# Optimization experiments

Hardware: AMD Instinct MI355X
Metric: run time of the kernel (lower is better)

Reference implementation:

```python
import math
import jax, jax.numpy as jnp
import numpy as np

HID = 2048      # hidden_size
NH = 16         # num_heads
KD = HID // NH  # key head dim = 128 (even, required by XPOS)
VD = HID        # value_dim (value_factor=1)
VHD = VD // NH  # value head dim
SCALE_BASE = 512
ROPE_BASE = 10000.0
GN_EPS = 1e-5


def _rotate_every_two(x):
    x1 = x[..., ::2]
    x2 = x[..., 1::2]
    return jnp.stack((-x2, x1), axis=-1).reshape(x.shape)


def _dup(a):  # repeat_interleave(x, 2, dim=-1)
    return jnp.repeat(a, 2, axis=-1)


def _xpos_apply(x, pos, inv_freq, xpos_scale, downscale):
    # x: [B, H, S, KD], pos: [B, S]
    posf = pos.astype(jnp.float32)
    angles = posf[:, :, None] * inv_freq[None, None, :]          # [B, S, KD/2]
    sin = _dup(jnp.sin(angles))[:, None]                          # [B, 1, S, KD]
    cos = _dup(jnp.cos(angles))[:, None]
    scale = xpos_scale[None, None, :] ** (posf[:, :, None] / SCALE_BASE)
    if downscale:
        scale = 1.0 / scale
    scale = _dup(scale)[:, None]                                  # [B, 1, S, KD]
    return (x * cos + _rotate_every_two(x) * sin) * scale


def setup_inputs() -> dict:
    key = jax.random.key(0)
    ks = jax.random.split(key, 6)
    B, S = 1, 2048
    std = 1.0 / HID
    x = jax.random.normal(ks[0], (B, S, HID), dtype=jnp.float32)
    position_ids = jnp.broadcast_to(jnp.arange(S, dtype=jnp.int64), (B, S))
    Wq = jax.random.normal(ks[1], (HID, HID), dtype=jnp.float32) * std
    Wk = jax.random.normal(ks[2], (HID, HID), dtype=jnp.float32) * std
    Wv = jax.random.normal(ks[3], (HID, VD), dtype=jnp.float32) * std
    Wg = jax.random.normal(ks[4], (HID, VD), dtype=jnp.float32) * std
    Wo = jax.random.normal(ks[5], (VD, HID), dtype=jnp.float32) * std
    gn_weight = jnp.ones((VD,), dtype=jnp.float32)
    gn_bias = jnp.zeros((VD,), dtype=jnp.float32)
    return {"x": x, "position_ids": position_ids, "Wq": Wq, "Wk": Wk,
            "Wv": Wv, "Wg": Wg, "Wo": Wo,
            "gn_weight": gn_weight, "gn_bias": gn_bias}


def reference(x, position_ids, Wq, Wk, Wv, Wg, Wo, gn_weight, gn_bias):
    B, S, _ = x.shape
    # XPOS / multiscale-decay buffers (deterministic, as in XPOSRelativePosition)
    inv_freq = 1.0 / (ROPE_BASE ** (jnp.arange(0, KD, 2, dtype=jnp.float32) / KD))
    xpos_scale = (jnp.arange(0, KD, 2, dtype=jnp.float32) + 0.4 * KD) / (1.4 * KD)
    gamma = 1.0 - jnp.exp(jnp.linspace(math.log(1.0 / 32), math.log(1.0 / 512), NH))
    log_gamma = jnp.log(gamma)                                    # [NH]

    # projections -> [B, H, S, d]
    q = (x @ Wq).reshape(B, S, NH, KD).transpose(0, 2, 1, 3)
    k = (x @ Wk).reshape(B, S, NH, KD).transpose(0, 2, 1, 3)
    v = (x @ Wv).reshape(B, S, NH, VHD).transpose(0, 2, 1, 3)
    g = x @ Wg                                                    # [B, S, VD]

    q = _xpos_apply(q, position_ids, inv_freq, xpos_scale, downscale=False)
    k = _xpos_apply(k, position_ids, inv_freq, xpos_scale, downscale=True)

    # decay mask: exp(log_gamma * (i-j)) for i>=j else 0   [B, H, S, S]
    relpos = position_ids[:, :, None] - position_ids[:, None, :]  # [B, S, S]
    decay = jnp.exp(log_gamma[None, :, None, None]
                    * jnp.maximum(relpos, 0)[:, None].astype(jnp.float32))
    decay = decay * (relpos >= 0)[:, None].astype(jnp.float32)

    scores = jnp.einsum('bhqd,bhkd->bhqk', q, k) * decay          # [B, H, S, S]
    retained = jnp.einsum('bhqk,bhkv->bhqv', scores, v)           # [B, H, S, VHD]

    # GroupNorm(num_heads, value_dim): normalize each head group per token
    r = retained.transpose(0, 2, 1, 3)                            # [B, S, H, VHD]
    mean = r.mean(axis=-1, keepdims=True)
    var = r.var(axis=-1, keepdims=True)
    rn = (r - mean) * jax.lax.rsqrt(var + GN_EPS)
    rn = rn * gn_weight.reshape(NH, VHD) + gn_bias.reshape(NH, VHD)
    rn = rn.reshape(B, S, VD)

    out = (jax.nn.silu(g) * rn) @ Wo                              # [B, S, HID]
    return out
```

## Files before the change

### kernel.cpp

```cpp
#include <hip/hip_runtime.h>
#include <math.h>

#define S_LEN 2048
#define HIDD  2048
#define NHEAD 16
#define HD    128

#define TILE_SH 4096

typedef __attribute__((ext_vector_type(8))) short short8;
typedef __attribute__((ext_vector_type(4))) float float4v;
typedef unsigned short ushort_t;

static __device__ __forceinline__ ushort_t f2bf(float f) {
    unsigned int u = __float_as_uint(f);
    u += 0x7fff + ((u >> 16) & 1);
    return (ushort_t)(u >> 16);
}
static __device__ __forceinline__ float bf2f(ushort_t s) {
    return __uint_as_float(((unsigned int)s) << 16);
}
__device__ __forceinline__ float silu_f(float x) { return x / (1.f + expf(-x)); }

__device__ __forceinline__ void gl_lds16(const ushort_t* g, short* l) {
    __builtin_amdgcn_global_load_lds((const __attribute__((address_space(1))) void*)g,
                                     (__attribute__((address_space(3))) void*)l, 16, 0, 0);
}

__global__ __launch_bounds__(256)
void split_kernel(const float* __restrict__ in, ushort_t* __restrict__ hi,
                  ushort_t* __restrict__ lo, int n4)
{
    const int i = blockIdx.x * 256 + threadIdx.x;
    if (i >= n4) return;
    const float4 v = ((const float4*)in)[i];
    ushort4 h, l;
    h.x = f2bf(v.x); l.x = f2bf(v.x - bf2f(h.x));
    h.y = f2bf(v.y); l.y = f2bf(v.y - bf2f(h.y));
    h.z = f2bf(v.z); l.z = f2bf(v.z - bf2f(h.z));
    h.w = f2bf(v.w); l.w = f2bf(v.w - bf2f(h.w));
    const int row = i >> 9, c4 = (i & 511) * 4;
    const size_t off = ((size_t)((row >> 7) * 64 + (c4 >> 5))) * TILE_SH
                     + (row & 127) * 32 + (c4 & 31);
    *(ushort4*)&hi[off] = h;
    *(ushort4*)&lo[off] = l;
}

__global__ __launch_bounds__(256)
void addp_kernel(float* __restrict__ out, const float* __restrict__ p, int n4)
{
    const int i = blockIdx.x * 256 + threadIdx.x;
    if (i >= n4) return;
    float4 a = ((const float4*)out)[i];
    const float4 b = ((const float4*)p)[i];
    a.x += b.x; a.y += b.y; a.z += b.z; a.w += b.w;
    ((float4*)out)[i] = a;
}

__global__ __launch_bounds__(256)
void split_transpose(const float* __restrict__ W, ushort_t* __restrict__ Thi,
                     ushort_t* __restrict__ Tlo)
{
    __shared__ float t[64][65];
    const int k0 = blockIdx.y * 64, n0 = blockIdx.x * 64;
    const int tx = threadIdx.x & 15, ty = threadIdx.x >> 4;
    #pragma unroll
    for (int it = 0; it < 4; it++) {
        const int k = ty + it * 16;
        const float4 v = *(const float4*)&W[(size_t)(k0 + k) * HIDD + n0 + tx * 4];
        t[k][tx * 4 + 0] = v.x; t[k][tx * 4 + 1] = v.y;
        t[k][tx * 4 + 2] = v.z; t[k][tx * 4 + 3] = v.w;
    }
    __syncthreads();
    #pragma unroll
    for (int it = 0; it < 4; it++) {
        const int n = ty + it * 16;
        ushort4 h, l; float a;
        a = t[tx * 4 + 0][n]; h.x = f2bf(a); l.x = f2bf(a - bf2f(h.x));
        a = t[tx * 4 + 1][n]; h.y = f2bf(a); l.y = f2bf(a - bf2f(h.y));
        a = t[tx * 4 + 2][n]; h.z = f2bf(a); l.z = f2bf(a - bf2f(h.z));
        a = t[tx * 4 + 3][n]; h.w = f2bf(a); l.w = f2bf(a - bf2f(h.w));
        const int nn_ = n0 + n, kk_ = k0 + tx * 4;
        const size_t off = ((size_t)((nn_ >> 7) * 64 + (kk_ >> 5))) * TILE_SH
                         + (nn_ & 127) * 32 + (kk_ & 31);
        *(ushort4*)&Thi[off] = h;
        *(ushort4*)&Tlo[off] = l;
    }
}

template<int MODE>
__global__ __launch_bounds__(256, 2)
void mfma_gemm(const ushort_t* __restrict__ Ahi, const ushort_t* __restrict__ Alo,
               const ushort_t* __restrict__ WT, const int* __restrict__ pos_ids,
               ushort_t* __restrict__ qhi, ushort_t* __restrict__ qlo,
               ushort_t* __restrict__ khi, ushort_t* __restrict__ klo,
               ushort_t* __restrict__ vThi, ushort_t* __restrict__ vTlo,
               float* __restrict__ gbuf, float* __restrict__ outC)
{
    __shared__ __align__(16) short sm[(MODE == 1) ? 32768 : 16384];

    const int tid = threadIdx.x;
    const int w = tid >> 6, L = tid & 63;
    const int qd = L >> 4, lc = L & 15;
    const int lin = blockIdx.x;
    int n0, m0, kh = 0;
    if (MODE == 0) {
        n0 = (((lin & 7) << 3) + ((lin >> 3) & 7)) << 7;
        m0 = (lin >> 6) << 7;
    } else {
        n0 = (lin & 15) << 7;
        m0 = ((lin >> 4) & 15) << 7;
        kh = lin >> 8;
    }
    const size_t PL = (size_t)HIDD * HIDD;

    int sel, nn;
    const ushort_t *Bhi, *Blo;
    if (MODE == 0) {
        sel = n0 >> 11; nn = n0 & 2047;
        Bhi = WT + (size_t)sel * 2 * PL; Blo = Bhi + PL;
    } else {
        sel = -1; nn = n0;
        Bhi = WT; Blo = WT + PL;
    }

    const ushort_t* pbase = (w == 0) ? Ahi : (w == 1) ? Alo : (w == 2) ? Bhi : Blo;
    const int rt = ((w < 2) ? m0 : nn) >> 7;
    const ushort_t* tb0 = pbase + (size_t)rt * 64 * TILE_SH + L * 8;

    const int wm = (w & 1) * 64, wn = (w >> 1) * 64;
    int aoff[4], boff[4];
    #pragma unroll
    for (int i = 0; i < 4; i++) aoff[i] = (wm + i * 16 + lc) * 32 + qd * 8;
    #pragma unroll
    for (int j = 0; j < 4; j++) boff[j] = (wn + j * 16 + lc) * 32 + qd * 8;

    float4v acc[4][4];
    #pragma unroll
    for (int i = 0; i < 4; i++)
        #pragma unroll
        for (int j = 0; j < 4; j++)
            #pragma unroll
            for (int r = 0; r < 4; r++) acc[i][j][r] = 0.f;

    const int kt0 = (MODE == 1) ? kh * 32 : 0;
    const int kt1 = (MODE == 1) ? kt0 + 32 : 64;

    if (MODE == 0) {
        short* ldsw = sm + w * 4096;
        for (int kt = kt0; kt < kt1; kt++) {
            const ushort_t* g = tb0 + (size_t)kt * TILE_SH;
            #pragma unroll
            for (int t = 0; t < 8; t++)
                gl_lds16(g + t * 512, ldsw + t * 512);
            __syncthreads();

            short8 bhf[4], blf[4];
            #pragma unroll
            for (int j = 0; j < 4; j++) {
                bhf[j] = *(const short8*)(sm + 8192  + boff[j]);
                blf[j] = *(const short8*)(sm + 12288 + boff[j]);
            }
            #pragma unroll
            for (int i = 0; i < 4; i++) {
                const short8 ahf = *(const short8*)(sm + aoff[i]);
                const short8 alf = *(const short8*)(sm + 4096 + aoff[i]);
                #pragma unroll
                for (int j = 0; j < 4; j++) {
                    acc[i][j] = __builtin_amdgcn_mfma_f32_16x16x32_bf16(ahf, bhf[j], acc[i][j], 0, 0, 0);
                    acc[i][j] = __builtin_amdgcn_mfma_f32_16x16x32_bf16(alf, bhf[j], acc[i][j], 0, 0, 0);
                    acc[i][j] = __builtin_amdgcn_mfma_f32_16x16x32_bf16(ahf, blf[j], acc[i][j], 0, 0, 0);
                }
            }
            __syncthreads();
        }
    } else {
        {
            const ushort_t* g = tb0 + (size_t)kt0 * TILE_SH;
            #pragma unroll
            for (int t = 0; t < 8; t++)
                gl_lds16(g + t * 512, sm + w * 4096 + t * 512);
            asm volatile("s_waitcnt vmcnt(0)" ::: "memory");
            __builtin_amdgcn_s_barrier();
            __builtin_amdgcn_sched_barrier(0);
        }
        int cur = 0;
        for (int kt = kt0; kt < kt1; kt++) {
            const short* cb = sm + (cur << 14);
            short* nb = sm + ((cur ^ 1) << 14);
            if (kt + 1 < kt1) {
                const ushort_t* g = tb0 + (size_t)(kt + 1) * TILE_SH;
                #pragma unroll
                for (int t = 0; t < 8; t++)
                    gl_lds16(g + t * 512, nb + w * 4096 + t * 512);
            }
            short8 bhf[4], blf[4];
            #pragma unroll
            for (int j = 0; j < 4; j++) {
                bhf[j] = *(const short8*)(cb + 8192  + boff[j]);
                blf[j] = *(const short8*)(cb + 12288 + boff[j]);
            }
            #pragma unroll
            for (int i = 0; i < 4; i++) {
                const short8 ahf = *(const short8*)(cb + aoff[i]);
                const short8 alf = *(const short8*)(cb + 4096 + aoff[i]);
                #pragma unroll
                for (int j = 0; j < 4; j++) {
                    acc[i][j] = __builtin_amdgcn_mfma_f32_16x16x32_bf16(ahf, bhf[j], acc[i][j], 0, 0, 0);
                    acc[i][j] = __builtin_amdgcn_mfma_f32_16x16x32_bf16(alf, bhf[j], acc[i][j], 0, 0, 0);
                    acc[i][j] = __builtin_amdgcn_mfma_f32_16x16x32_bf16(ahf, blf[j], acc[i][j], 0, 0, 0);
                }
            }
            asm volatile("s_waitcnt vmcnt(0)" ::: "memory");
            __builtin_amdgcn_s_barrier();
            __builtin_amdgcn_sched_barrier(0);
            cur ^= 1;
        }
    }

    float* ob = (float*)sm;
    const int half = w & 1;
    const int head = nn >> 7;

    #pragma unroll
    for (int i = 0; i < 4; i++) {
        #pragma unroll
        for (int j = 0; j < 4; j++)
            #pragma unroll
            for (int r = 0; r < 4; r++)
                ob[(half * 16 + qd * 4 + r) * 132 + wn + j * 16 + lc] = acc[i][j][r];
        __syncthreads();

        if (MODE == 1 || sel == 3) {
            float* dst = (MODE == 1) ? (kh ? gbuf : outC) : gbuf;
            #pragma unroll
            for (int p = 0; p < 4; p++) {
                const int row = p * 8 + (tid >> 5);
                const int c = (tid & 31) * 4;
                const int grow = m0 + (row >> 4) * 64 + i * 16 + (row & 15);
                const float4 vv = *(const float4*)&ob[row * 132 + c];
                *(float4*)&dst[(size_t)grow * HIDD + nn + c] = vv;
            }
        } else if (sel == 2) {
            const int d = tid >> 1, hs = tid & 1;
            const int sbase = m0 + hs * 64 + i * 16;
            short8 h0, h1, l0, l1;
            #pragma unroll
            for (int sp = 0; sp < 8; sp++) {
                float a = ob[(hs * 16 + sp) * 132 + d];
                ushort_t hb = f2bf(a);
                h0[sp] = (short)hb; l0[sp] = (short)f2bf(a - bf2f(hb));
                a = ob[(hs * 16 + 8 + sp) * 132 + d];
                hb = f2bf(a);
                h1[sp] = (short)hb; l1[sp] = (short)f2bf(a - bf2f(hb));
            }
            ushort_t* dh = vThi + ((size_t)head * HD + d) * S_LEN + sbase;
            ushort_t* dl = vTlo + ((size_t)head * HD + d) * S_LEN + sbase;
            *(short8*)dh = h0; *(short8*)(dh + 8) = h1;
            *(short8*)dl = l0; *(short8*)(dl + 8) = l1;
        } else {
            const float sgn = (sel == 0) ? 1.f : -1.f;
            ushort_t* dhb = (sel == 0) ? qhi : khi;
            ushort_t* dlb = (sel == 0) ? qlo : klo;
            #pragma unroll
            for (int p = 0; p < 2; p++) {
                const int row = p * 16 + (tid >> 4);
                const int c8 = (tid & 15) * 8;
                const int grow = m0 + (row >> 4) * 64 + i * 16 + (row & 15);
                const float pos = (float)pos_ids[grow];
                const float pe = sgn * pos * (1.f / 512.f);
                short8 hv, lv;
                #pragma unroll
                for (int pp = 0; pp < 4; pp++) {
                    const int d = c8 + pp * 2;
                    const float v0 = ob[row * 132 + d], v1 = ob[row * 132 + d + 1];
                    const float invf = exp2f(-(float)d * (13.28771238f / 128.f));
                    float s, c_; sincosf(pos * invf, &s, &c_);
                    const float scl = exp2f(log2f(((float)d + 51.2f) * (1.f / 179.2f)) * pe);
                    const float e0 = (v0 * c_ - v1 * s) * scl;
                    const float e1 = (v1 * c_ + v0 * s) * scl;
                    const ushort_t h0 = f2bf(e0), h1 = f2bf(e1);
                    hv[pp * 2] = (short)h0;  hv[pp * 2 + 1] = (short)h1;
                    lv[pp * 2] = (short)f2bf(e0 - bf2f(h0));
                    lv[pp * 2 + 1] = (short)f2bf(e1 - bf2f(h1));
                }
                *(short8*)&dhb[((size_t)head * S_LEN + grow) * HD + c8] = hv;
                *(short8*)&dlb[((size_t)head * S_LEN + grow) * HD + c8] = lv;
            }
        }
        __syncthreads();
    }
}

#define KROW 136
#define VROW 40
#define KH_  0
#define KL_  (32 * KROW)
#define VH_  (2 * 32 * KROW)
#define VL_  (VH_ + 128 * VROW)
#define PH_  (VH_ + 2 * 128 * VROW)
#define PLO_ (PH_ + 64 * VROW)
#define YH_  8704
#define YL_  (YH_ + 64 * KROW)
__global__ __launch_bounds__(256, 2)
void retention2(const ushort_t* __restrict__ qhi, const ushort_t* __restrict__ qlo,
                const ushort_t* __restrict__ khi, const ushort_t* __restrict__ klo,
                const ushort_t* __restrict__ vThi, const ushort_t* __restrict__ vTlo,
                const float* __restrict__ gbuf, const float* __restrict__ gnw,
                const float* __restrict__ gnb,
                ushort_t* __restrict__ yhi, ushort_t* __restrict__ ylo)
{
    __shared__ __align__(16) short sm[26112];

    const int h = blockIdx.y;
    const int qb = (gridDim.x - 1) - blockIdx.x;
    const int r0 = qb * 64;
    const int tid = threadIdx.x;
    const int w = tid >> 6, L = tid & 63;
    const int qd = L >> 4, lc = L & 15;

    const float e = -3.4657359f + (float)h * ((-6.2383246f + 3.4657359f) / 15.f);
    const float lg2g = logf(1.f - expf(e)) * 1.44269504f;

    short8 qfh[4], qfl[4];
    {
        const size_t qb0 = ((size_t)h * S_LEN + r0 + w * 16 + lc) * HD + qd * 8;
        #pragma unroll
        for (int ks = 0; ks < 4; ks++) {
            qfh[ks] = *(const short8*)(qhi + qb0 + ks * 32);
            qfl[ks] = *(const short8*)(qlo + qb0 + ks * 32);
        }
    }

    float4v osum[2][4];
    #pragma unroll
    for (int mt = 0; mt < 2; mt++)
        #pragma unroll
        for (int j = 0; j < 4; j++)
            #pragma unroll
            for (int r = 0; r < 4; r++) osum[mt][j][r] = 0.f;

    const int qh_ = w >> 1, vh_ = w & 1;
    const int nch = (r0 + 64) / 32;

    for (int ch = 0; ch < nch; ch++) {
        const int kg0 = ch * 32;
        #pragma unroll
        for (int t = 0; t < 4; t++) {
            const int c = t * 256 + tid;
            const int p = c >> 9, r = (c >> 4) & 31, qq = c & 15;
            const ushort_t* src = (p ? klo : khi) + ((size_t)h * S_LEN + kg0 + r) * HD + qq * 8;
            *(short8*)(sm + (p ? KL_ : KH_) + r * KROW + qq * 8) = *(const short8*)src;
        }
        #pragma unroll
        for (int t = 0; t < 4; t++) {
            const int c = t * 256 + tid;
            const int p = c >> 9, r = (c >> 2) & 127, qq = c & 3;
            const ushort_t* src = (p ? vTlo : vThi) + ((size_t)h * HD + r) * S_LEN + kg0 + qq * 8;
            *(short8*)(sm + (p ? VL_ : VH_) + r * VROW + qq * 8) = *(const short8*)src;
        }
        __syncthreads();

        float4v sacc[2];
        #pragma unroll
        for (int j = 0; j < 2; j++)
            #pragma unroll
            for (int r = 0; r < 4; r++) sacc[j][r] = 0.f;
        #pragma unroll
        for (int ks = 0; ks < 4; ks++) {
            #pragma unroll
            for (int j = 0; j < 2; j++) {
                const short8 bh = *(const short8*)(sm + KH_ + (j * 16 + lc) * KROW + ks * 32 + qd * 8);
                const short8 bl = *(const short8*)(sm + KL_ + (j * 16 + lc) * KROW + ks * 32 + qd * 8);
                sacc[j] = __builtin_amdgcn_mfma_f32_16x16x32_bf16(qfh[ks], bh, sacc[j], 0, 0, 0);
                sacc[j] = __builtin_amdgcn_mfma_f32_16x16x32_bf16(qfl[ks], bh, sacc[j], 0, 0, 0);
                sacc[j] = __builtin_amdgcn_mfma_f32_16x16x32_bf16(qfh[ks], bl, sacc[j], 0, 0, 0);
            }
        }
        #pragma unroll
        for (int j = 0; j < 2; j++)
            #pragma unroll
            for (int r = 0; r < 4; r++) {
                const int dq = (r0 + w * 16 + qd * 4 + r) - (kg0 + j * 16 + lc);
                const float p = (dq >= 0) ? sacc[j][r] * exp2f(lg2g * (float)dq) : 0.f;
                const ushort_t hb = f2bf(p);
                const int off = (w * 16 + qd * 4 + r) * VROW + j * 16 + lc;
                sm[PH_ + off]  = (short)hb;
                sm[PLO_ + off] = (short)f2bf(p - bf2f(hb));
            }
        __syncthreads();

        #pragma unroll
        for (int mt = 0; mt < 2; mt++) {
            const short8 pfh = *(const short8*)(sm + PH_  + (qh_ * 32 + mt * 16 + lc) * VROW + qd * 8);
            const short8 pfl = *(const short8*)(sm + PLO_ + (qh_ * 32 + mt * 16 + lc) * VROW + qd * 8);
            #pragma unroll
            for (int j = 0; j < 4; j++) {
                const short8 vfh = *(const short8*)(sm + VH_ + (vh_ * 64 + j * 16 + lc) * VROW + qd * 8);
                const short8 vfl = *(const short8*)(sm + VL_ + (vh_ * 64 + j * 16 + lc) * VROW + qd * 8);
                osum[mt][j] = __builtin_amdgcn_mfma_f32_16x16x32_bf16(pfh, vfh, osum[mt][j], 0, 0, 0);
                osum[mt][j] = __builtin_amdgcn_mfma_f32_16x16x32_bf16(pfl, vfh, osum[mt][j], 0, 0, 0);
                osum[mt][j] = __builtin_amdgcn_mfma_f32_16x16x32_bf16(pfh, vfl, osum[mt][j], 0, 0, 0);
            }
        }
        __syncthreads();
    }

    float* fr = (float*)sm;
    #pragma unroll
    for (int mt = 0; mt < 2; mt++)
        #pragma unroll
        for (int r = 0; r < 4; r++) {
            float s1 = 0.f, s2 = 0.f;
            #pragma unroll
            for (int j = 0; j < 4; j++) { const float v = osum[mt][j][r]; s1 += v; s2 += v * v; }
            const int row = qh_ * 32 + mt * 16 + qd * 4 + r;
            fr[row * 32 + vh_ * 16 + lc] = s1;
            fr[2048 + row * 32 + vh_ * 16 + lc] = s2;
        }
    __syncthreads();
    if (tid < 64) {
        float s1 = 0.f, s2 = 0.f;
        #pragma unroll
        for (int t = 0; t < 32; t++) { s1 += fr[tid * 32 + t]; s2 += fr[2048 + tid * 32 + t]; }
        const float mean = s1 * (1.f / 128.f);
        const float var  = s2 * (1.f / 128.f) - mean * mean;
        fr[4096 + tid] = mean;
        fr[4160 + tid] = 1.f / sqrtf(var + 1e-5f);
    }
    __syncthreads();

    #pragma unroll
    for (int mt = 0; mt < 2; mt++)
        #pragma unroll
        for (int r = 0; r < 4; r++) {
            const int row = qh_ * 32 + mt * 16 + qd * 4 + r;
            const float mean = fr[4096 + row], inv = fr[4160 + row];
            const int grow = r0 + row;
            #pragma unroll
            for (int j = 0; j < 4; j++) {
                const int col = vh_ * 64 + j * 16 + lc;
                const float gv = gbuf[(size_t)grow * HIDD + h * HD + col];
                const float o = ((osum[mt][j][r] - mean) * inv * gnw[h * HD + col]
                                 + gnb[h * HD + col]) * silu_f(gv);
                const ushort_t hb = f2bf(o);
                sm[YH_ + row * KROW + col] = (short)hb;
                sm[YL_ + row * KROW + col] = (short)f2bf(o - bf2f(hb));
            }
        }
    __syncthreads();
    {
        const int r_ = tid >> 2, cs = (tid & 3) * 32;
        const int grow = r0 + r_;
        const size_t tb = ((size_t)((grow >> 7) * 64 + h * 4 + (tid & 3))) * TILE_SH
                        + (grow & 127) * 32;
        #pragma unroll
        for (int c8 = 0; c8 < 4; c8++) {
            *(short8*)(yhi + tb + c8 * 8) = *(const short8*)(sm + YH_ + r_ * KROW + cs + c8 * 8);
            *(short8*)(ylo + tb + c8 * 8) = *(const short8*)(sm + YL_ + r_ * KROW + cs + c8 * 8);
        }
    }
}

extern "C" void kernel_launch(void* const* d_in, const int* in_sizes, int n_in,
                              void* d_out, int out_size, void* d_ws, size_t ws_size,
                              hipStream_t stream) {
    const float* x   = (const float*)d_in[0];
    const int*   pid = (const int*)d_in[1];
    const float* W[5] = {(const float*)d_in[2], (const float*)d_in[3], (const float*)d_in[4],
                         (const float*)d_in[5], (const float*)d_in[6]};
    const float* gnw = (const float*)d_in[7];
    const float* gnb = (const float*)d_in[8];
    float* out = (float*)d_out;
    (void)in_sizes; (void)n_in; (void)out_size; (void)ws_size;

    const size_t PL = (size_t)HIDD * HIDD;

    ushort_t* wt   = (ushort_t*)d_ws;
    ushort_t* xhi  = wt + 10 * PL;
    ushort_t* xlo  = xhi + PL;
    ushort_t* qhi_ = xlo + PL;
    ushort_t* qlo_ = qhi_ + PL;
    ushort_t* khi_ = qlo_ + PL;
    ushort_t* klo_ = khi_ + PL;
    ushort_t* vThi = klo_ + PL;
    ushort_t* vTlo = vThi + PL;
    float*    gbuf = (float*)(vTlo + PL);
    ushort_t* yhi  = (ushort_t*)(gbuf + PL);
    ushort_t* ylo  = yhi + PL;
    float*    p1   = (float*)xhi;

    split_kernel<<<(int)(PL / 4 / 256), 256, 0, stream>>>(x, xhi, xlo, (int)(PL / 4));
    for (int m = 0; m < 5; m++)
        split_transpose<<<dim3(32, 32), 256, 0, stream>>>(W[m], wt + (size_t)m * 2 * PL,
                                                          wt + (size_t)m * 2 * PL + PL);

    mfma_gemm<0><<<1024, 256, 0, stream>>>(xhi, xlo, wt, pid,
        qhi_, qlo_, khi_, klo_, vThi, vTlo, gbuf, nullptr);

    retention2<<<dim3(32, 16), 256, 0, stream>>>(qhi_, qlo_, khi_, klo_, vThi, vTlo,
        gbuf, gnw, gnb, yhi, ylo);

    mfma_gemm<1><<<512, 256, 0, stream>>>(yhi, ylo, wt + 8 * PL, pid,
        nullptr, nullptr, nullptr, nullptr, nullptr, nullptr, p1, out);

    addp_kernel<<<(int)(PL / 4 / 256), 256, 0, stream>>>(out, p1, (int)(PL / 4));
}
```

Before: 559.1 us.

## Load GEMM A fragments from global directly, shrink LDS, batch weight transposes

```diff
diff --git a/kernel.cpp b/kernel.cpp
--- a/kernel.cpp
+++ b/kernel.cpp
@@ -58,10 +58,17 @@
 }
 
 __global__ __launch_bounds__(256)
-void split_transpose(const float* __restrict__ W, ushort_t* __restrict__ Thi,
-                     ushort_t* __restrict__ Tlo)
+void split_transpose_all(const float* __restrict__ W0, const float* __restrict__ W1,
+                         const float* __restrict__ W2, const float* __restrict__ W3,
+                         const float* __restrict__ W4, ushort_t* __restrict__ wt)
 {
     __shared__ float t[64][65];
+    const size_t PL = (size_t)HIDD * HIDD;
+    const int z = blockIdx.z;
+    const float* W = (z == 0) ? W0 : (z == 1) ? W1 : (z == 2) ? W2 : (z == 3) ? W3 : W4;
+    ushort_t* Thi = wt + (size_t)z * 2 * PL;
+    ushort_t* Tlo = Thi + PL;
+
     const int k0 = blockIdx.y * 64, n0 = blockIdx.x * 64;
     const int tx = threadIdx.x & 15, ty = threadIdx.x >> 4;
     #pragma unroll
@@ -95,9 +102,9 @@
                ushort_t* __restrict__ qhi, ushort_t* __restrict__ qlo,
                ushort_t* __restrict__ khi, ushort_t* __restrict__ klo,
                ushort_t* __restrict__ vThi, ushort_t* __restrict__ vTlo,
-               float* __restrict__ gbuf, float* __restrict__ outC)
+               float* __restrict__ gbuf, float* __restrict__ outC, int mbase)
 {
-    __shared__ __align__(16) short sm[(MODE == 1) ? 32768 : 16384];
+    __shared__ __align__(16) short sm[(MODE == 1) ? 16896 : 8448];
 
     const int tid = threadIdx.x;
     const int w = tid >> 6, L = tid & 63;
@@ -106,7 +113,7 @@
     int n0, m0, kh = 0;
     if (MODE == 0) {
         n0 = (((lin & 7) << 3) + ((lin >> 3) & 7)) << 7;
-        m0 = (lin >> 6) << 7;
+        m0 = mbase + ((lin >> 6) << 7);
     } else {
         n0 = (lin & 15) << 7;
         m0 = ((lin >> 4) & 15) << 7;
@@ -124,9 +131,12 @@
         Bhi = WT; Blo = WT + PL;
     }
 
-    const ushort_t* pbase = (w == 0) ? Ahi : (w == 1) ? Alo : (w == 2) ? Bhi : Blo;
-    const int rt = ((w < 2) ? m0 : nn) >> 7;
-    const ushort_t* tb0 = pbase + (size_t)rt * 64 * TILE_SH + L * 8;
+    const int sdoff = (w >> 1) * 4096 + (w & 1) * 2048 + L * 8;
+    const ushort_t* sbase = ((w < 2) ? Bhi : Blo) + (size_t)(nn >> 7) * 64 * TILE_SH
+                          + (w & 1) * 2048 + L * 8;
+
+    const ushort_t* aTh = Ahi + (size_t)(m0 >> 7) * 64 * TILE_SH;
+    const ushort_t* aTl = Alo + (size_t)(m0 >> 7) * 64 * TILE_SH;
 
     const int wm = (w & 1) * 64, wn = (w >> 1) * 64;
     int aoff[4], boff[4];
@@ -147,70 +157,74 @@
     const int kt1 = (MODE == 1) ? kt0 + 32 : 64;
 
     if (MODE == 0) {
-        short* ldsw = sm + w * 4096;
         for (int kt = kt0; kt < kt1; kt++) {
-            const ushort_t* g = tb0 + (size_t)kt * TILE_SH;
-            #pragma unroll
-            for (int t = 0; t < 8; t++)
-                gl_lds16(g + t * 512, ldsw + t * 512);
+            const size_t ko = (size_t)kt * TILE_SH;
+            short8 ahf[4], alf[4];
+            #pragma unroll
+            for (int i = 0; i < 4; i++) {
+                ahf[i] = *(const short8*)(aTh + ko + aoff[i]);
+                alf[i] = *(const short8*)(aTl + ko + aoff[i]);
+            }
+            #pragma unroll
+            for (int t = 0; t < 4; t++)
+                gl_lds16(sbase + ko + t * 512, sm + sdoff + t * 512);
             __syncthreads();
 
             short8 bhf[4], blf[4];
             #pragma unroll
             for (int j = 0; j < 4; j++) {
-                bhf[j] = *(const short8*)(sm + 8192  + boff[j]);
-                blf[j] = *(const short8*)(sm + 12288 + boff[j]);
-            }
-            #pragma unroll
-            for (int i = 0; i < 4; i++) {
-                const short8 ahf = *(const short8*)(sm + aoff[i]);
-                const short8 alf = *(const short8*)(sm + 4096 + aoff[i]);
+                bhf[j] = *(const short8*)(sm + boff[j]);
+                blf[j] = *(const short8*)(sm + 4096 + boff[j]);
+            }
+            #pragma unroll
+            for (int i = 0; i < 4; i++)
                 #pragma unroll
                 for (int j = 0; j < 4; j++) {
-                    acc[i][j] = __builtin_amdgcn_mfma_f32_16x16x32_bf16(ahf, bhf[j], acc[i][j], 0, 0, 0);
-                    acc[i][j] = __builtin_amdgcn_mfma_f32_16x16x32_bf16(alf, bhf[j], acc[i][j], 0, 0, 0);
-                    acc[i][j] = __builtin_amdgcn_mfma_f32_16x16x32_bf16(ahf, blf[j], acc[i][j], 0, 0, 0);
+                    acc[i][j] = __builtin_amdgcn_mfma_f32_16x16x32_bf16(ahf[i], bhf[j], acc[i][j], 0, 0, 0);
+                    acc[i][j] = __builtin_amdgcn_mfma_f32_16x16x32_bf16(alf[i], bhf[j], acc[i][j], 0, 0, 0);
+                    acc[i][j] = __builtin_amdgcn_mfma_f32_16x16x32_bf16(ahf[i], blf[j], acc[i][j], 0, 0, 0);
                 }
-            }
             __syncthreads();
         }
     } else {
-        {
-            const ushort_t* g = tb0 + (size_t)kt0 * TILE_SH;
-            #pragma unroll
-            for (int t = 0; t < 8; t++)
-                gl_lds16(g + t * 512, sm + w * 4096 + t * 512);
-            asm volatile("s_waitcnt vmcnt(0)" ::: "memory");
-            __builtin_amdgcn_s_barrier();
-            __builtin_amdgcn_sched_barrier(0);
-        }
+        #pragma unroll
+        for (int t = 0; t < 4; t++)
+            gl_lds16(sbase + (size_t)kt0 * TILE_SH + t * 512, sm + sdoff + t * 512);
+        asm volatile("s_waitcnt vmcnt(0)" ::: "memory");
+        __builtin_amdgcn_s_barrier();
+        __builtin_amdgcn_sched_barrier(0);
+
         int cur = 0;
         for (int kt = kt0; kt < kt1; kt++) {
-            const short* cb = sm + (cur << 14);
-            short* nb = sm + ((cur ^ 1) << 14);
             if (kt + 1 < kt1) {
-                const ushort_t* g = tb0 + (size_t)(kt + 1) * TILE_SH;
+                const size_t kn = (size_t)(kt + 1) * TILE_SH;
+                short* nb = sm + (cur ^ 1) * 8192;
                 #pragma unroll
-                for (int t = 0; t < 8; t++)
-                    gl_lds16(g + t * 512, nb + w * 4096 + t * 512);
-            }
+                for (int t = 0; t < 4; t++)
+                    gl_lds16(sbase + kn + t * 512, nb + sdoff + t * 512);
+            }
+            const size_t ko = (size_t)kt * TILE_SH;
+            short8 ahf[4], alf[4];
+            #pragma unroll
+            for (int i = 0; i < 4; i++) {
+                ahf[i] = *(const short8*)(aTh + ko + aoff[i]);
+                alf[i] = *(const short8*)(aTl + ko + aoff[i]);
+            }
+            const short* cb = sm + cur * 8192;
             short8 bhf[4], blf[4];
             #pragma unroll
             for (int j = 0; j < 4; j++) {
-                bhf[j] = *(const short8*)(cb + 8192  + boff[j]);
-                blf[j] = *(const short8*)(cb + 12288 + boff[j]);
-            }
-            #pragma unroll
-            for (int i = 0; i < 4; i++) {
-                const short8 ahf = *(const short8*)(cb + aoff[i]);
-                const short8 alf = *(const short8*)(cb + 4096 + aoff[i]);
+                bhf[j] = *(const short8*)(cb + boff[j]);
+                blf[j] = *(const short8*)(cb + 4096 + boff[j]);
+            }
+            #pragma unroll
+            for (int i = 0; i < 4; i++)
                 #pragma unroll
                 for (int j = 0; j < 4; j++) {
-                    acc[i][j] = __builtin_amdgcn_mfma_f32_16x16x32_bf16(ahf, bhf[j], acc[i][j], 0, 0, 0);
-                    acc[i][j] = __builtin_amdgcn_mfma_f32_16x16x32_bf16(alf, bhf[j], acc[i][j], 0, 0, 0);
-                    acc[i][j] = __builtin_amdgcn_mfma_f32_16x16x32_bf16(ahf, blf[j], acc[i][j], 0, 0, 0);
+                    acc[i][j] = __builtin_amdgcn_mfma_f32_16x16x32_bf16(ahf[i], bhf[j], acc[i][j], 0, 0, 0);
+                    acc[i][j] = __builtin_amdgcn_mfma_f32_16x16x32_bf16(alf[i], bhf[j], acc[i][j], 0, 0, 0);
+                    acc[i][j] = __builtin_amdgcn_mfma_f32_16x16x32_bf16(ahf[i], blf[j], acc[i][j], 0, 0, 0);
                 }
-            }
             asm volatile("s_waitcnt vmcnt(0)" ::: "memory");
             __builtin_amdgcn_s_barrier();
             __builtin_amdgcn_sched_barrier(0);
@@ -243,7 +257,7 @@
             }
         } else if (sel == 2) {
             const int d = tid >> 1, hs = tid & 1;
-            const int sbase = m0 + hs * 64 + i * 16;
+            const int sbase2 = m0 + hs * 64 + i * 16;
             short8 h0, h1, l0, l1;
             #pragma unroll
             for (int sp = 0; sp < 8; sp++) {
@@ -254,8 +268,8 @@
                 hb = f2bf(a);
                 h1[sp] = (short)hb; l1[sp] = (short)f2bf(a - bf2f(hb));
             }
-            ushort_t* dh = vThi + ((size_t)head * HD + d) * S_LEN + sbase;
-            ushort_t* dl = vTlo + ((size_t)head * HD + d) * S_LEN + sbase;
+            ushort_t* dh = vThi + ((size_t)head * HD + d) * S_LEN + sbase2;
+            ushort_t* dl = vTlo + ((size_t)head * HD + d) * S_LEN + sbase2;
             *(short8*)dh = h0; *(short8*)(dh + 8) = h1;
             *(short8*)dl = l0; *(short8*)(dl + 8) = l1;
         } else {
@@ -467,8 +481,6 @@
                               hipStream_t stream) {
     const float* x   = (const float*)d_in[0];
     const int*   pid = (const int*)d_in[1];
-    const float* W[5] = {(const float*)d_in[2], (const float*)d_in[3], (const float*)d_in[4],
-                         (const float*)d_in[5], (const float*)d_in[6]};
     const float* gnw = (const float*)d_in[7];
     const float* gnb = (const float*)d_in[8];
     float* out = (float*)d_out;
@@ -491,18 +503,20 @@
     float*    p1   = (float*)xhi;
 
     split_kernel<<<(int)(PL / 4 / 256), 256, 0, stream>>>(x, xhi, xlo, (int)(PL / 4));
-    for (int m = 0; m < 5; m++)
-        split_transpose<<<dim3(32, 32), 256, 0, stream>>>(W[m], wt + (size_t)m * 2 * PL,
-                                                          wt + (size_t)m * 2 * PL + PL);
-
-    mfma_gemm<0><<<1024, 256, 0, stream>>>(xhi, xlo, wt, pid,
-        qhi_, qlo_, khi_, klo_, vThi, vTlo, gbuf, nullptr);
+    split_transpose_all<<<dim3(32, 32, 5), 256, 0, stream>>>(
+        (const float*)d_in[2], (const float*)d_in[3], (const float*)d_in[4],
+        (const float*)d_in[5], (const float*)d_in[6], wt);
+
+    mfma_gemm<0><<<512, 256, 0, stream>>>(xhi, xlo, wt, pid,
+        qhi_, qlo_, khi_, klo_, vThi, vTlo, gbuf, nullptr, 0);
+    mfma_gemm<0><<<512, 256, 0, stream>>>(xhi, xlo, wt, pid,
+        qhi_, qlo_, khi_, klo_, vThi, vTlo, gbuf, nullptr, 1024);
 
     retention2<<<dim3(32, 16), 256, 0, stream>>>(qhi_, qlo_, khi_, klo_, vThi, vTlo,
         gbuf, gnw, gnb, yhi, ylo);
 
     mfma_gemm<1><<<512, 256, 0, stream>>>(yhi, ylo, wt + 8 * PL, pid,
-        nullptr, nullptr, nullptr, nullptr, nullptr, nullptr, p1, out);
+        nullptr, nullptr, nullptr, nullptr, nullptr, nullptr, p1, out, 0);
 
     addp_kernel<<<(int)(PL / 4 / 256), 256, 0, stream>>>(out, p1, (int)(PL / 4));
 }
```

Result: no change. 553.1 us (-1.1%).
